# Kernel optimization log

Measured on AMD Instinct MI355X. Metric: run time of the kernel, lower is better.

The kernel has to match this reference:

```python
import jax, jax.numpy as jnp
import numpy as np

B, C, H, W = 4, 512, 56, 56
G, K = 16, 3
P = K * K
GC = C // G
DWK = 3
PAD = 1
OFFSET_SCALE = 1.0


def setup_inputs():
    key = jax.random.key(0)
    ks = jax.random.split(key, 10)

    def w(i, shape, sc=0.02):
        return jax.random.normal(ks[i], shape, jnp.float32) * sc

    return {
        "x": jax.random.normal(ks[0], (B, C, H, W), jnp.float32),
        "w_in": w(1, (C, C)), "b_in": jnp.zeros((C,), jnp.float32),
        "w_dw": w(2, (DWK, DWK, 1, C)), "b_dw": jnp.zeros((C,), jnp.float32),
        "ln_g": jnp.ones((C,), jnp.float32), "ln_b": jnp.zeros((C,), jnp.float32),
        "w_off": w(3, (C, G * P * 2)), "b_off": jnp.zeros((G * P * 2,), jnp.float32),
        "w_mask": w(4, (C, G * P)), "b_mask": jnp.zeros((G * P,), jnp.float32),
        "w_out": w(5, (C, C)), "b_out": jnp.zeros((C,), jnp.float32),
        "bn_g": jnp.ones((C,), jnp.float32), "bn_b": jnp.zeros((C,), jnp.float32),
        "bn_m": w(6, (C,), 0.1), "bn_v": jnp.abs(w(7, (C,), 0.1)) + 1.0,
    }


def _dcnv3_core(xp, offset, mask):
    """xp: [B,H,W,C]; offset: [B,H,W,G*P*2]; mask (softmaxed over P): [B,H,W,G,P]."""
    xpad = jnp.pad(xp, ((0, 0), (PAD, PAD), (PAD, PAD), (0, 0)))
    Hin, Win = H + 2 * PAD, W + 2 * PAD
    # normalized reference points (output-location centers in padded input coords)
    ref_x = (jnp.arange(W, dtype=jnp.float32) + 0.5 + (K - 1) // 2) / Win
    ref_y = (jnp.arange(H, dtype=jnp.float32) + 0.5 + (K - 1) // 2) / Hin
    # dilation grid, kx-major / ky-minor flattening (matches InternImage core)
    k = jnp.arange(K, dtype=jnp.float32) - (K - 1) // 2
    gx = jnp.repeat(k, K) / Win  # [P]
    gy = jnp.tile(k, K) / Hin    # [P]
    off = offset.reshape(B, H, W, G, P, 2)
    lx = ref_x[None, None, :, None, None] + gx * OFFSET_SCALE + off[..., 0] * OFFSET_SCALE / Win
    ly = ref_y[None, :, None, None, None] + gy * OFFSET_SCALE + off[..., 1] * OFFSET_SCALE / Hin
    # grid_sample semantics, align_corners=False, zero padding
    px = lx * Win - 0.5
    py = ly * Hin - 0.5
    x0f = jnp.floor(px)
    y0f = jnp.floor(py)
    tx = px - x0f
    ty = py - y0f
    x0 = x0f.astype(jnp.int32)
    y0 = y0f.astype(jnp.int32)
    flat = xpad.reshape(B, Hin * Win * G, GC)
    gidx = jnp.arange(G)[None, None, :, None]

    def corner(fb, yi, xi):
        valid = (yi >= 0) & (yi < Hin) & (xi >= 0) & (xi < Win)
        idx = (jnp.clip(yi, 0, Hin - 1) * Win + jnp.clip(xi, 0, Win - 1)) * G + gidx
        return jnp.take(fb, idx, axis=0) * valid[..., None]  # [H,W,G,P,GC]

    def sample_one(fb, y0b, x0b, tyb, txb):
        w00 = ((1 - tyb) * (1 - txb))[..., None]
        w01 = ((1 - tyb) * txb)[..., None]
        w10 = (tyb * (1 - txb))[..., None]
        w11 = (tyb * txb)[..., None]
        return (corner(fb, y0b, x0b) * w00 + corner(fb, y0b, x0b + 1) * w01
                + corner(fb, y0b + 1, x0b) * w10 + corner(fb, y0b + 1, x0b + 1) * w11)

    samp = jax.vmap(sample_one)(flat, y0, x0, ty, tx)  # [B,H,W,G,P,GC]
    return jnp.einsum('bhwgpc,bhwgp->bhwgc', samp, mask).reshape(B, H, W, C)


def reference(x, w_in, b_in, w_dw, b_dw, ln_g, ln_b, w_off, b_off, w_mask, b_mask, w_out, b_out, bn_g, bn_b, bn_m, bn_v):
    xh = jnp.transpose(x, (0, 2, 3, 1))  # NCHW -> NHWC
    xp = xh @ w_in + b_in                # input_proj
    # offset/mask branch: depthwise conv + LayerNorm(channels) + GELU
    x1 = jax.lax.conv_general_dilated(xh, w_dw, (1, 1), 'SAME', feature_group_count=C,
                                      dimension_numbers=('NHWC', 'HWIO', 'NHWC')) + b_dw
    mu = x1.mean(-1, keepdims=True)
    var = x1.var(-1, keepdims=True)
    x1 = (x1 - mu) / jnp.sqrt(var + 1e-6) * ln_g + ln_b
    x1 = jax.nn.gelu(x1, approximate=False)
    offset = x1 @ w_off + b_off
    mask = jax.nn.softmax((x1 @ w_mask + b_mask).reshape(B, H, W, G, P), axis=-1)
    y = _dcnv3_core(xp, offset, mask)
    y = y @ w_out + b_out                # output_proj
    y = jnp.transpose(y, (0, 3, 1, 2))   # NHWC -> NCHW
    # BatchNorm2d (inference: running stats) + SiLU
    y = (y - bn_m[:, None, None]) / jnp.sqrt(bn_v[:, None, None] + 1e-5) * bn_g[:, None, None] + bn_b[:, None, None]
    return jax.nn.silu(y)
```

## Files before the change

### kernel.cpp

```cpp
#include <hip/hip_runtime.h>
#include <cmath>

constexpr int B_ = 4, C_ = 512, H_ = 56, W_ = 56;
constexpr int HW_ = H_ * W_;
constexpr int NPIX = B_ * HW_;
constexpr int G_ = 16, P_ = 9;
constexpr int NMSK = G_ * P_;
constexpr int GEMM_BLOCKS = 392;

typedef __attribute__((ext_vector_type(8))) short short8;
typedef __attribute__((ext_vector_type(4))) float f32x4;

__device__ __forceinline__ float b2f(ushort u) {
    union { unsigned int i; float f; } v; v.i = (unsigned int)u << 16; return v.f;
}
__device__ __forceinline__ ushort f2b(float f) {
    unsigned int x = __float_as_uint(f);
    unsigned int r = (x + 0x7fffu + ((x >> 16) & 1u)) >> 16;
    return (ushort)r;
}
__device__ __forceinline__ void gload16(const ushort* g, ushort* l) {
    __builtin_amdgcn_global_load_lds(
        (const __attribute__((address_space(1))) unsigned int*)g,
        (__attribute__((address_space(3))) unsigned int*)l, 16, 0, 0);
}

union GemmSMem {
    struct { ushort As[128 * 64]; ushort Bs[128 * 64]; } s;
    float eb[4][32][67];
};

__global__ __launch_bounds__(256) void prep_weights_kernel(
    const float* __restrict__ w_in, const float* __restrict__ w_off,
    const float* __restrict__ w_mask, const float* __restrict__ w_out,
    const float* __restrict__ b_off, const float* __restrict__ b_mask,
    ushort* __restrict__ wtA, ushort* __restrict__ wtOM, ushort* __restrict__ wtO,
    float* __restrict__ bOM)
{
    __shared__ float tile[32][33];
    int z = blockIdx.z;
    int k0 = blockIdx.x * 32;
    int n0 = blockIdx.y * 32;
    int tx = threadIdx.x, ty = threadIdx.y;
    for (int i = ty; i < 32; i += 8) {
        int k = k0 + i, n = n0 + tx;
        float v;
        if (z == 0) v = w_in[k * 512 + n];
        else if (z == 1) v = w_out[k * 512 + n];
        else v = (n < 288) ? w_off[k * 288 + n]
                           : (n < 432 ? w_mask[k * 144 + (n - 288)] : 0.f);
        tile[i][tx] = v;
    }
    __syncthreads();
    ushort* dst = (z == 0) ? wtA : (z == 1 ? wtO : wtOM);
    for (int i = ty; i < 32; i += 8)
        dst[(size_t)(n0 + i) * 512 + k0 + tx] = f2b(tile[tx][i]);
    if (z == 2 && blockIdx.x == 0 && blockIdx.y == 0) {
        int t = ty * 32 + tx;
        for (int tt = t; tt < 512; tt += 256)
            bOM[tt] = (tt < 288) ? b_off[tt] : (tt < 432 ? b_mask[tt - 288] : 0.f);
    }
}

__global__ __launch_bounds__(256) void transpose_in_kernel(
    const float* __restrict__ in, ushort* __restrict__ out)
{
    __shared__ float tile[32][33];
    int b = blockIdx.z;
    int hw0 = blockIdx.x * 32;
    int c0 = blockIdx.y * 32;
    int tx = threadIdx.x, ty = threadIdx.y;
    const float* ib = in + (size_t)b * C_ * HW_;
    #pragma unroll
    for (int i = ty; i < 32; i += 8)
        tile[i][tx] = ib[(size_t)(c0 + i) * HW_ + hw0 + tx];
    __syncthreads();
    ushort* ob = out + (size_t)b * HW_ * C_;
    #pragma unroll
    for (int i = ty; i < 32; i += 8)
        ob[(size_t)(hw0 + i) * C_ + c0 + tx] = f2b(tile[tx][i]);
}

template <int MODE>
__device__ __forceinline__ void gemm_body(
    ushort* __restrict__ As, ushort* __restrict__ Bs, float* __restrict__ ebf,
    int wgid, const ushort* __restrict__ A, const ushort* __restrict__ Bt,
    const float* __restrict__ bias, void* __restrict__ Cout,
    const float* __restrict__ bng, const float* __restrict__ bnb,
    const float* __restrict__ bnm, const float* __restrict__ bnv)
{
    int tid = threadIdx.x;
    int lane = tid & 63, wid = tid >> 6;
    int row0 = (wgid >> 2) * 128, col0 = (wgid & 3) * 128;
    int wm = wid >> 1, wn = wid & 1;

    f32x4 acc[4][4] = {};

    int lr = lane >> 3;
    int sc = (lane & 7) ^ lr;

    for (int k0 = 0; k0 < 512; k0 += 64) {
        if (k0) __syncthreads();
        #pragma unroll
        for (int i = 0; i < 4; i++) {
            int rb = (wid * 4 + i) * 8;
            gload16(A + (size_t)(row0 + rb + lr) * 512 + k0 + sc * 8, &As[rb * 64]);
            gload16(Bt + (size_t)(col0 + rb + lr) * 512 + k0 + sc * 8, &Bs[rb * 64]);
        }
        __syncthreads();
        #pragma unroll
        for (int ks = 0; ks < 2; ks++) {
            short8 af[4], bf[4];
            #pragma unroll
            for (int mi = 0; mi < 4; mi++) {
                int r = wm * 64 + mi * 16 + (lane & 15);
                int c = ((lane >> 4) + ks * 4) ^ (r & 7);
                af[mi] = *(const short8*)((const char*)As + r * 128 + c * 16);
            }
            #pragma unroll
            for (int ni = 0; ni < 4; ni++) {
                int r = wn * 64 + ni * 16 + (lane & 15);
                int c = ((lane >> 4) + ks * 4) ^ (r & 7);
                bf[ni] = *(const short8*)((const char*)Bs + r * 128 + c * 16);
            }
            #pragma unroll
            for (int mi = 0; mi < 4; mi++)
                #pragma unroll
                for (int ni = 0; ni < 4; ni++)
                    acc[mi][ni] = __builtin_amdgcn_mfma_f32_16x16x32_bf16(
                        af[mi], bf[ni], acc[mi][ni], 0, 0, 0);
        }
    }

    if constexpr (MODE == 2) {
        __syncthreads();
        int n_lane = row0 + wm * 64 + lane;
        int bb = n_lane / HW_;
        int hww = n_lane - bb * HW_;
        size_t obase = (size_t)bb * C_ * HW_ + hww;
        #pragma unroll
        for (int half = 0; half < 2; half++) {
            #pragma unroll
            for (int ni2 = 0; ni2 < 2; ni2++) {
                int ni = half * 2 + ni2;
                int col = col0 + wn * 64 + ni * 16 + (lane & 15);
                float bv = bias[col];
                float inv = rsqrtf(bnv[col] + 1e-5f);
                float bsc = bng[col] * inv;
                float bsh = bnb[col] - bnm[col] * bsc;
                int cl = ni2 * 16 + (lane & 15);
                int rl = (lane >> 4) * 4;
                #pragma unroll
                for (int mi = 0; mi < 4; mi++)
                    #pragma unroll
                    for (int r = 0; r < 4; r++) {
                        float val = acc[mi][ni][r] + bv;
                        float t2 = val * bsc + bsh;
                        float s = t2 / (1.f + expf(-t2));
                        ebf[((wid * 32) + cl) * 67 + mi * 16 + rl + r] = s;
                    }
            }
            __syncthreads();
            #pragma unroll
            for (int c = 0; c < 32; c++) {
                int chan = col0 + wn * 64 + half * 32 + c;
                ((float*)Cout)[obase + (size_t)chan * HW_] =
                    ebf[((wid * 32) + c) * 67 + lane];
            }
            __syncthreads();
        }
    } else {
        #pragma unroll
        for (int ni = 0; ni < 4; ni++) {
            int col = col0 + wn * 64 + ni * 16 + (lane & 15);
            float bv = bias[col];
            #pragma unroll
            for (int mi = 0; mi < 4; mi++) {
                int rowb = row0 + wm * 64 + mi * 16 + (lane >> 4) * 4;
                #pragma unroll
                for (int r = 0; r < 4; r++) {
                    float val = acc[mi][ni][r] + bv;
                    if constexpr (MODE == 0)
                        ((float*)Cout)[(size_t)(rowb + r) * 512 + col] = val;
                    else
                        ((ushort*)Cout)[(size_t)(rowb + r) * 512 + col] = f2b(val);
                }
            }
        }
    }
}

template <int MODE>
__global__ __launch_bounds__(256) void mfma_gemm_kernel(
    const ushort* __restrict__ A, const ushort* __restrict__ Bt,
    const float* __restrict__ bias, void* __restrict__ Cout,
    const float* __restrict__ bng, const float* __restrict__ bnb,
    const float* __restrict__ bnm, const float* __restrict__ bnv)
{
    __shared__ GemmSMem sm;
    int bid = blockIdx.x;
    int wgid = (bid & 7) * 49 + (bid >> 3);
    gemm_body<MODE>(sm.s.As, sm.s.Bs, &sm.eb[0][0][0], wgid,
                    A, Bt, bias, Cout, bng, bnb, bnm, bnv);
}

__device__ __forceinline__ void dwln_body(
    int bid, const ushort* __restrict__ xh, const float* __restrict__ wdw,
    const float* __restrict__ bdw, const float* __restrict__ lng,
    const float* __restrict__ lnb, ushort* __restrict__ x1)
{
    int tid = threadIdx.x;
    int wid = tid >> 6, lane = tid & 63;
    int j = (bid & 7) * (NPIX / 32) + (bid >> 3);
    int n = j * 4 + wid;
    int b = n / HW_, hw = n % HW_;
    int h = hw / W_, w = hw % W_;
    int c0 = lane * 8;
    const ushort* base = xh + (size_t)b * HW_ * C_ + c0;

    uint4 nb[9];
    #pragma unroll
    for (int ky = 0; ky < 3; ky++)
        #pragma unroll
        for (int kx = 0; kx < 3; kx++) {
            int hh = h + ky - 1, ww = w + kx - 1;
            bool ok = (hh >= 0) & (hh < H_) & (ww >= 0) & (ww < W_);
            nb[ky * 3 + kx] = ok ? *(const uint4*)(base + ((size_t)hh * W_ + ww) * C_)
                                 : make_uint4(0u, 0u, 0u, 0u);
        }

    float acc[8];
    {
        float4 b0 = *(const float4*)&bdw[c0];
        float4 b1 = *(const float4*)&bdw[c0 + 4];
        acc[0] = b0.x; acc[1] = b0.y; acc[2] = b0.z; acc[3] = b0.w;
        acc[4] = b1.x; acc[5] = b1.y; acc[6] = b1.z; acc[7] = b1.w;
    }
    #pragma unroll
    for (int p = 0; p < 9; p++) {
        float4 w0 = *(const float4*)&wdw[p * C_ + c0];
        float4 w1 = *(const float4*)&wdw[p * C_ + c0 + 4];
        float wv[8] = {w0.x, w0.y, w0.z, w0.w, w1.x, w1.y, w1.z, w1.w};
        unsigned int u[4] = {nb[p].x, nb[p].y, nb[p].z, nb[p].w};
        #pragma unroll
        for (int q = 0; q < 4; q++) {
            float lo = __uint_as_float(u[q] << 16);
            float hi = __uint_as_float(u[q] & 0xffff0000u);
            acc[2 * q]     += wv[2 * q]     * lo;
            acc[2 * q + 1] += wv[2 * q + 1] * hi;
        }
    }

    float s1 = 0.f, s2 = 0.f;
    #pragma unroll
    for (int q = 0; q < 8; q++) { s1 += acc[q]; s2 += acc[q] * acc[q]; }
    #pragma unroll
    for (int o = 32; o > 0; o >>= 1) {
        s1 += __shfl_xor(s1, o);
        s2 += __shfl_xor(s2, o);
    }
    float mean = s1 * (1.f / 512.f);
    float var = s2 * (1.f / 512.f) - mean * mean;
    float inv = rsqrtf(var + 1e-6f);

    float4 g0 = *(const float4*)&lng[c0];
    float4 g1 = *(const float4*)&lng[c0 + 4];
    float4 e0 = *(const float4*)&lnb[c0];
    float4 e1 = *(const float4*)&lnb[c0 + 4];
    float gv[8] = {g0.x, g0.y, g0.z, g0.w, g1.x, g1.y, g1.z, g1.w};
    float ev[8] = {e0.x, e0.y, e0.z, e0.w, e1.x, e1.y, e1.z, e1.w};
    unsigned int outw[4];
    #pragma unroll
    for (int q = 0; q < 4; q++) {
        float t0 = (acc[2 * q]     - mean) * inv * gv[2 * q]     + ev[2 * q];
        float t1 = (acc[2 * q + 1] - mean) * inv * gv[2 * q + 1] + ev[2 * q + 1];
        float ge0 = 0.5f * t0 * (1.f + erff(t0 * 0.70710678118654752f));
        float ge1 = 0.5f * t1 * (1.f + erff(t1 * 0.70710678118654752f));
        outw[q] = (unsigned int)f2b(ge0) | ((unsigned int)f2b(ge1) << 16);
    }
    *(uint4*)&x1[(size_t)n * C_ + c0] = make_uint4(outw[0], outw[1], outw[2], outw[3]);
}

__global__ __launch_bounds__(256) void g1_dwln_kernel(
    const ushort* __restrict__ xh, const ushort* __restrict__ wtA,
    const float* __restrict__ b_in, ushort* __restrict__ xpb,
    const float* __restrict__ wdw, const float* __restrict__ bdw,
    const float* __restrict__ lng, const float* __restrict__ lnb,
    ushort* __restrict__ x1)
{
    __shared__ GemmSMem sm;
    int bid = blockIdx.x;
    if (bid < GEMM_BLOCKS) {
        int wgid = (bid & 7) * 49 + (bid >> 3);
        gemm_body<1>(sm.s.As, sm.s.Bs, &sm.eb[0][0][0], wgid,
                     xh, wtA, b_in, xpb, nullptr, nullptr, nullptr, nullptr);
    } else {
        dwln_body(bid - GEMM_BLOCKS, xh, wdw, bdw, lng, lnb, x1);
    }
}

__global__ __launch_bounds__(256) void dcn_sample_kernel(
    const ushort* __restrict__ xp, const ushort* __restrict__ om,
    ushort* __restrict__ y1)
{
    __shared__ float slog[NMSK];
    __shared__ float sw4[NMSK][4];
    __shared__ int   sa4[NMSK][4];
    int bid = blockIdx.x;
    int n = (bid & 7) * (NPIX / 8) + (bid >> 3);
    int b = n / HW_, hw = n % HW_;
    int h = hw / W_, w = hw % W_;
    int tid = threadIdx.x;
    const ushort* omp = om + (size_t)n * 512;

    if (tid < NMSK) slog[tid] = b2f(omp[288 + tid]);
    __syncthreads();
    if (tid < G_) {
        float mx = -1e30f;
        #pragma unroll
        for (int p = 0; p < P_; p++) mx = fmaxf(mx, slog[tid * P_ + p]);
        float e[P_], s = 0.f;
        #pragma unroll
        for (int p = 0; p < P_; p++) { e[p] = expf(slog[tid * P_ + p] - mx); s += e[p]; }
        float invs = 1.f / s;
        #pragma unroll
        for (int p = 0; p < P_; p++) slog[tid * P_ + p] = e[p] * invs;
    }
    __syncthreads();
    if (tid < NMSK) {
        int g = tid / 9, p = tid - g * 9;
        float ox = b2f(omp[g * 18 + p * 2 + 0]);
        float oy = b2f(omp[g * 18 + p * 2 + 1]);
        float px = (float)(w + (p / 3)) + ox;
        float py = (float)(h + (p % 3)) + oy;
        float x0f = floorf(px), y0f = floorf(py);
        float tx = px - x0f, ty = py - y0f;
        int x0 = (int)x0f, y0 = (int)y0f;
        float m = slog[tid];
        float ww[4] = { (1.f - ty) * (1.f - tx) * m, (1.f - ty) * tx * m,
                        ty * (1.f - tx) * m,         ty * tx * m };
        #pragma unroll
        for (int i = 0; i < 4; i++) {
            int yy = y0 + (i >> 1), xx = x0 + (i & 1);
            bool valid = (yy >= 1 && yy <= H_ && xx >= 1 && xx <= W_);
            sa4[tid][i] = valid ? ((yy - 1) * W_ + (xx - 1)) * C_ : 0;
            sw4[tid][i] = valid ? ww[i] : 0.f;
        }
    }
    __syncthreads();

    const ushort* xpb = xp + (size_t)b * HW_ * C_;
    int c0 = tid * 2;
    int g = tid >> 4;

    int addr[P_][4];
    #pragma unroll
    for (int p = 0; p < P_; p++)
        #pragma unroll
        for (int i = 0; i < 4; i++)
            addr[p][i] = sa4[g * 9 + p][i] + c0;

    unsigned int v[P_][4];
    #pragma unroll
    for (int p = 0; p < P_; p++)
        #pragma unroll
        for (int i = 0; i < 4; i++)
            v[p][i] = *(const unsigned int*)(xpb + addr[p][i]);

    float ax = 0.f, ay = 0.f;
    #pragma unroll
    for (int p = 0; p < P_; p++)
        #pragma unroll
        for (int i = 0; i < 4; i++) {
            float wgt = sw4[g * 9 + p][i];
            float lo = __uint_as_float(v[p][i] << 16);
            float hi = __uint_as_float(v[p][i] & 0xffff0000u);
            ax += wgt * lo;
            ay += wgt * hi;
        }

    ushort2 o; o.x = f2b(ax); o.y = f2b(ay);
    *(ushort2*)&y1[(size_t)n * 512 + c0] = o;
}

extern "C" void kernel_launch(void* const* d_in, const int* in_sizes, int n_in,
                              void* d_out, int out_size, void* d_ws, size_t ws_size,
                              hipStream_t stream)
{
    const float* x      = (const float*)d_in[0];
    const float* w_in   = (const float*)d_in[1];
    const float* b_in   = (const float*)d_in[2];
    const float* w_dw   = (const float*)d_in[3];
    const float* b_dw   = (const float*)d_in[4];
    const float* ln_g   = (const float*)d_in[5];
    const float* ln_b   = (const float*)d_in[6];
    const float* w_off  = (const float*)d_in[7];
    const float* b_off  = (const float*)d_in[8];
    const float* w_mask = (const float*)d_in[9];
    const float* b_mask = (const float*)d_in[10];
    const float* w_out  = (const float*)d_in[11];
    const float* b_out  = (const float*)d_in[12];
    const float* bn_g   = (const float*)d_in[13];
    const float* bn_b   = (const float*)d_in[14];
    const float* bn_m   = (const float*)d_in[15];
    const float* bn_v   = (const float*)d_in[16];
    float* out = (float*)d_out;

    const size_t NC = (size_t)NPIX * C_;
    char* wsp = (char*)d_ws;
    ushort* xh  = (ushort*)wsp;  wsp += NC * 2;
    ushort* x1  = (ushort*)wsp;  wsp += NC * 2;
    ushort* xpb = (ushort*)wsp;  wsp += NC * 2;
    ushort* om  = (ushort*)wsp;  wsp += NC * 2;
    ushort* wtA = (ushort*)wsp;  wsp += 512 * 512 * 2;
    ushort* wtOM= (ushort*)wsp;  wsp += 512 * 512 * 2;
    ushort* wtO = (ushort*)wsp;  wsp += 512 * 512 * 2;
    float*  bOM = (float*)wsp;   wsp += 512 * 4;

    dim3 tb(32, 8);
    prep_weights_kernel<<<dim3(16, 16, 3), tb, 0, stream>>>(
        w_in, w_off, w_mask, w_out, b_off, b_mask, wtA, wtOM, wtO, bOM);

    transpose_in_kernel<<<dim3(HW_ / 32, C_ / 32, B_), tb, 0, stream>>>(x, xh);

    g1_dwln_kernel<<<GEMM_BLOCKS + NPIX / 4, 256, 0, stream>>>(
        xh, wtA, b_in, xpb, w_dw, b_dw, ln_g, ln_b, x1);

    mfma_gemm_kernel<1><<<GEMM_BLOCKS, 256, 0, stream>>>(
        x1, wtOM, bOM, om, nullptr, nullptr, nullptr, nullptr);

    dcn_sample_kernel<<<NPIX, 256, 0, stream>>>(xpb, om, x1 );

    mfma_gemm_kernel<2><<<GEMM_BLOCKS, 256, 0, stream>>>(
        x1, wtO, b_out, out, bn_g, bn_b, bn_m, bn_v);
}
```

Baseline: 112.0 us.

## Shrink GEMM tiles to 64x64 and merge weight prep with input transpose

The bf16 MFMA GEMMs move from 128x128 to 64x64 output tiles, so each GEMM launches 1568 blocks instead of 392. This gives better occupancy and load balance across the CUs, and the MODE 2 epilogue is simplified into a single LDS staging pass. Separately, the weight-prep and input-transpose kernels are fused into one launch to save a kernel launch. The cost is less operand reuse per block, so each GEMM reads more global and L2 data.

```diff
diff --git a/kernel.cpp b/kernel.cpp
--- a/kernel.cpp
+++ b/kernel.cpp
@@ -6,7 +6,9 @@
 constexpr int NPIX = B_ * HW_;
 constexpr int G_ = 16, P_ = 9;
 constexpr int NMSK = G_ * P_;
-constexpr int GEMM_BLOCKS = 392;
+constexpr int GEMM_BLOCKS = 1568;
+constexpr int TRANS_BLOCKS = (HW_ / 32) * (C_ / 32) * B_;
+constexpr int PREP_BLOCKS = 16 * 16 * 3;
 
 typedef __attribute__((ext_vector_type(8))) short short8;
 typedef __attribute__((ext_vector_type(4))) float f32x4;
@@ -26,11 +28,12 @@
 }
 
 union GemmSMem {
-    struct { ushort As[128 * 64]; ushort Bs[128 * 64]; } s;
-    float eb[4][32][67];
+    struct { ushort As[64 * 64]; ushort Bs[64 * 64]; } s;
+    float eb[64 * 67];
 };
 
-__global__ __launch_bounds__(256) void prep_weights_kernel(
+__global__ __launch_bounds__(256) void pre_kernel(
+    const float* __restrict__ x, ushort* __restrict__ xh,
     const float* __restrict__ w_in, const float* __restrict__ w_off,
     const float* __restrict__ w_mask, const float* __restrict__ w_out,
     const float* __restrict__ b_off, const float* __restrict__ b_mask,
@@ -38,47 +41,49 @@
     float* __restrict__ bOM)
 {
     __shared__ float tile[32][33];
-    int z = blockIdx.z;
-    int k0 = blockIdx.x * 32;
-    int n0 = blockIdx.y * 32;
+    int bid = blockIdx.x;
     int tx = threadIdx.x, ty = threadIdx.y;
-    for (int i = ty; i < 32; i += 8) {
-        int k = k0 + i, n = n0 + tx;
-        float v;
-        if (z == 0) v = w_in[k * 512 + n];
-        else if (z == 1) v = w_out[k * 512 + n];
-        else v = (n < 288) ? w_off[k * 288 + n]
-                           : (n < 432 ? w_mask[k * 144 + (n - 288)] : 0.f);
-        tile[i][tx] = v;
-    }
-    __syncthreads();
-    ushort* dst = (z == 0) ? wtA : (z == 1 ? wtO : wtOM);
-    for (int i = ty; i < 32; i += 8)
-        dst[(size_t)(n0 + i) * 512 + k0 + tx] = f2b(tile[tx][i]);
-    if (z == 2 && blockIdx.x == 0 && blockIdx.y == 0) {
-        int t = ty * 32 + tx;
-        for (int tt = t; tt < 512; tt += 256)
-            bOM[tt] = (tt < 288) ? b_off[tt] : (tt < 432 ? b_mask[tt - 288] : 0.f);
-    }
-}
-
-__global__ __launch_bounds__(256) void transpose_in_kernel(
-    const float* __restrict__ in, ushort* __restrict__ out)
-{
-    __shared__ float tile[32][33];
-    int b = blockIdx.z;
-    int hw0 = blockIdx.x * 32;
-    int c0 = blockIdx.y * 32;
-    int tx = threadIdx.x, ty = threadIdx.y;
-    const float* ib = in + (size_t)b * C_ * HW_;
-    #pragma unroll
-    for (int i = ty; i < 32; i += 8)
-        tile[i][tx] = ib[(size_t)(c0 + i) * HW_ + hw0 + tx];
-    __syncthreads();
-    ushort* ob = out + (size_t)b * HW_ * C_;
-    #pragma unroll
-    for (int i = ty; i < 32; i += 8)
-        ob[(size_t)(hw0 + i) * C_ + c0 + tx] = f2b(tile[tx][i]);
+    if (bid < TRANS_BLOCKS) {
+        int bx = bid % 98;
+        int rem = bid / 98;
+        int by = rem % 16;
+        int bz = rem / 16;
+        int hw0 = bx * 32, c0 = by * 32;
+        const float* ib = x + (size_t)bz * C_ * HW_;
+        #pragma unroll
+        for (int i = ty; i < 32; i += 8)
+            tile[i][tx] = ib[(size_t)(c0 + i) * HW_ + hw0 + tx];
+        __syncthreads();
+        ushort* ob = xh + (size_t)bz * HW_ * C_;
+        #pragma unroll
+        for (int i = ty; i < 32; i += 8)
+            ob[(size_t)(hw0 + i) * C_ + c0 + tx] = f2b(tile[tx][i]);
+    } else {
+        int p = bid - TRANS_BLOCKS;
+        int px = p % 16;
+        int py = (p / 16) % 16;
+        int pz = p / 256;
+        int k0 = px * 32;
+        int n0 = py * 32;
+        for (int i = ty; i < 32; i += 8) {
+            int k = k0 + i, n = n0 + tx;
+            float v;
+            if (pz == 0) v = w_in[k * 512 + n];
+            else if (pz == 1) v = w_out[k * 512 + n];
+            else v = (n < 288) ? w_off[k * 288 + n]
+                               : (n < 432 ? w_mask[k * 144 + (n - 288)] : 0.f);
+            tile[i][tx] = v;
+        }
+        __syncthreads();
+        ushort* dst = (pz == 0) ? wtA : (pz == 1 ? wtO : wtOM);
+        for (int i = ty; i < 32; i += 8)
+            dst[(size_t)(n0 + i) * 512 + k0 + tx] = f2b(tile[tx][i]);
+        if (pz == 2 && px == 0 && py == 0) {
+            int t = ty * 32 + tx;
+            for (int tt = t; tt < 512; tt += 256)
+                bOM[tt] = (tt < 288) ? b_off[tt] : (tt < 432 ? b_mask[tt - 288] : 0.f);
+        }
+    }
 }
 
 template <int MODE>
@@ -91,10 +96,10 @@
 {
     int tid = threadIdx.x;
     int lane = tid & 63, wid = tid >> 6;
-    int row0 = (wgid >> 2) * 128, col0 = (wgid & 3) * 128;
+    int row0 = (wgid >> 3) * 64, col0 = (wgid & 7) * 64;
     int wm = wid >> 1, wn = wid & 1;
 
-    f32x4 acc[4][4] = {};
+    f32x4 acc[2][2] = {};
 
     int lr = lane >> 3;
     int sc = (lane & 7) ^ lr;
@@ -102,31 +107,31 @@
     for (int k0 = 0; k0 < 512; k0 += 64) {
         if (k0) __syncthreads();
         #pragma unroll
-        for (int i = 0; i < 4; i++) {
-            int rb = (wid * 4 + i) * 8;
-            gload16(A + (size_t)(row0 + rb + lr) * 512 + k0 + sc * 8, &As[rb * 64]);
-            gload16(Bt + (size_t)(col0 + rb + lr) * 512 + k0 + sc * 8, &Bs[rb * 64]);
+        for (int i = 0; i < 2; i++) {
+            int s = wid * 2 + i;
+            gload16(A + (size_t)(row0 + s * 8 + lr) * 512 + k0 + sc * 8, &As[s * 512]);
+            gload16(Bt + (size_t)(col0 + s * 8 + lr) * 512 + k0 + sc * 8, &Bs[s * 512]);
         }
         __syncthreads();
         #pragma unroll
         for (int ks = 0; ks < 2; ks++) {
-            short8 af[4], bf[4];
+            short8 af[2], bf[2];
             #pragma unroll
-            for (int mi = 0; mi < 4; mi++) {
-                int r = wm * 64 + mi * 16 + (lane & 15);
+            for (int mi = 0; mi < 2; mi++) {
+                int r = wm * 32 + mi * 16 + (lane & 15);
                 int c = ((lane >> 4) + ks * 4) ^ (r & 7);
                 af[mi] = *(const short8*)((const char*)As + r * 128 + c * 16);
             }
             #pragma unroll
-            for (int ni = 0; ni < 4; ni++) {
-                int r = wn * 64 + ni * 16 + (lane & 15);
+            for (int ni = 0; ni < 2; ni++) {
+                int r = wn * 32 + ni * 16 + (lane & 15);
                 int c = ((lane >> 4) + ks * 4) ^ (r & 7);
                 bf[ni] = *(const short8*)((const char*)Bs + r * 128 + c * 16);
             }
             #pragma unroll
-            for (int mi = 0; mi < 4; mi++)
+            for (int mi = 0; mi < 2; mi++)
                 #pragma unroll
-                for (int ni = 0; ni < 4; ni++)
+                for (int ni = 0; ni < 2; ni++)
                     acc[mi][ni] = __builtin_amdgcn_mfma_f32_16x16x32_bf16(
                         af[mi], bf[ni], acc[mi][ni], 0, 0, 0);
         }
@@ -134,49 +139,42 @@
 
     if constexpr (MODE == 2) {
         __syncthreads();
-        int n_lane = row0 + wm * 64 + lane;
-        int bb = n_lane / HW_;
-        int hww = n_lane - bb * HW_;
-        size_t obase = (size_t)bb * C_ * HW_ + hww;
-        #pragma unroll
-        for (int half = 0; half < 2; half++) {
+        #pragma unroll
+        for (int ni = 0; ni < 2; ni++) {
+            int cl = wn * 32 + ni * 16 + (lane & 15);
+            int col = col0 + cl;
+            float bv = bias[col];
+            float inv = rsqrtf(bnv[col] + 1e-5f);
+            float bsc = bng[col] * inv;
+            float bsh = bnb[col] - bnm[col] * bsc;
+            int rl = (lane >> 4) * 4;
             #pragma unroll
-            for (int ni2 = 0; ni2 < 2; ni2++) {
-                int ni = half * 2 + ni2;
-                int col = col0 + wn * 64 + ni * 16 + (lane & 15);
-                float bv = bias[col];
-                float inv = rsqrtf(bnv[col] + 1e-5f);
-                float bsc = bng[col] * inv;
-                float bsh = bnb[col] - bnm[col] * bsc;
-                int cl = ni2 * 16 + (lane & 15);
-                int rl = (lane >> 4) * 4;
+            for (int mi = 0; mi < 2; mi++)
                 #pragma unroll
-                for (int mi = 0; mi < 4; mi++)
-                    #pragma unroll
-                    for (int r = 0; r < 4; r++) {
-                        float val = acc[mi][ni][r] + bv;
-                        float t2 = val * bsc + bsh;
-                        float s = t2 / (1.f + expf(-t2));
-                        ebf[((wid * 32) + cl) * 67 + mi * 16 + rl + r] = s;
-                    }
-            }
-            __syncthreads();
-            #pragma unroll
-            for (int c = 0; c < 32; c++) {
-                int chan = col0 + wn * 64 + half * 32 + c;
-                ((float*)Cout)[obase + (size_t)chan * HW_] =
-                    ebf[((wid * 32) + c) * 67 + lane];
-            }
-            __syncthreads();
+                for (int r = 0; r < 4; r++) {
+                    float val = acc[mi][ni][r] + bv;
+                    float t2 = val * bsc + bsh;
+                    float s = t2 / (1.f + expf(-t2));
+                    ebf[cl * 67 + wm * 32 + mi * 16 + rl + r] = s;
+                }
+        }
+        __syncthreads();
+        int bb = row0 / HW_;
+        int hw0 = row0 - bb * HW_;
+        float* ob = (float*)Cout + (size_t)bb * C_ * HW_ + hw0 + lane;
+        #pragma unroll
+        for (int it = 0; it < 16; it++) {
+            int chan = it * 4 + wid;
+            ob[(size_t)(col0 + chan) * HW_] = ebf[chan * 67 + lane];
         }
     } else {
         #pragma unroll
-        for (int ni = 0; ni < 4; ni++) {
-            int col = col0 + wn * 64 + ni * 16 + (lane & 15);
+        for (int ni = 0; ni < 2; ni++) {
+            int col = col0 + wn * 32 + ni * 16 + (lane & 15);
             float bv = bias[col];
             #pragma unroll
-            for (int mi = 0; mi < 4; mi++) {
-                int rowb = row0 + wm * 64 + mi * 16 + (lane >> 4) * 4;
+            for (int mi = 0; mi < 2; mi++) {
+                int rowb = row0 + wm * 32 + mi * 16 + (lane >> 4) * 4;
                 #pragma unroll
                 for (int r = 0; r < 4; r++) {
                     float val = acc[mi][ni][r] + bv;
@@ -199,8 +197,8 @@
 {
     __shared__ GemmSMem sm;
     int bid = blockIdx.x;
-    int wgid = (bid & 7) * 49 + (bid >> 3);
-    gemm_body<MODE>(sm.s.As, sm.s.Bs, &sm.eb[0][0][0], wgid,
+    int wgid = (bid & 7) * (GEMM_BLOCKS / 8) + (bid >> 3);
+    gemm_body<MODE>(sm.s.As, sm.s.Bs, sm.eb, wgid,
                     A, Bt, bias, Cout, bng, bnb, bnm, bnv);
 }
 
@@ -291,8 +289,8 @@
     __shared__ GemmSMem sm;
     int bid = blockIdx.x;
     if (bid < GEMM_BLOCKS) {
-        int wgid = (bid & 7) * 49 + (bid >> 3);
-        gemm_body<1>(sm.s.As, sm.s.Bs, &sm.eb[0][0][0], wgid,
+        int wgid = (bid & 7) * (GEMM_BLOCKS / 8) + (bid >> 3);
+        gemm_body<1>(sm.s.As, sm.s.Bs, sm.eb, wgid,
                      xh, wtA, b_in, xpb, nullptr, nullptr, nullptr, nullptr);
     } else {
         dwln_body(bid - GEMM_BLOCKS, xh, wdw, bdw, lng, lnb, x1);
@@ -418,10 +416,8 @@
     float*  bOM = (float*)wsp;   wsp += 512 * 4;
 
     dim3 tb(32, 8);
-    prep_weights_kernel<<<dim3(16, 16, 3), tb, 0, stream>>>(
-        w_in, w_off, w_mask, w_out, b_off, b_mask, wtA, wtOM, wtO, bOM);
-
-    transpose_in_kernel<<<dim3(HW_ / 32, C_ / 32, B_), tb, 0, stream>>>(x, xh);
+    pre_kernel<<<TRANS_BLOCKS + PREP_BLOCKS, tb, 0, stream>>>(
+        x, xh, w_in, w_off, w_mask, w_out, b_off, b_mask, wtA, wtOM, wtO, bOM);
 
     g1_dwln_kernel<<<GEMM_BLOCKS + NPIX / 4, 256, 0, stream>>>(
         xh, wtA, b_in, xpb, w_dw, b_dw, ln_g, ln_b, x1);
```

Result: faster. 108.2 us (-3.4%).
